# Performance work log

Measured on AMD Instinct MI355X. Metric: run time of the kernel, lower is better.

## Reference

```python
import jax, jax.numpy as jnp
import numpy as np

B, N, DIM, H = 8, 4096, 768, 12
HD = DIM // H
SCALE = HD ** -0.5


def setup_inputs() -> dict:
    key = jax.random.key(0)
    ks = jax.random.split(key, 6)
    x = jax.random.normal(ks[0], (B, N, DIM), dtype=jnp.float32)
    # torch nn.Linear weights: [out_features, in_features]
    Wqkv = jax.random.normal(ks[1], (3 * DIM, DIM), dtype=jnp.float32) * (DIM ** -0.5)
    Wp = jax.random.normal(ks[2], (DIM, DIM), dtype=jnp.float32) * (DIM ** -0.5)
    bp = jnp.zeros((DIM,), dtype=jnp.float32)
    w_q = jax.random.normal(ks[3], (H, HD), dtype=jnp.float32)
    w_k = jax.random.normal(ks[4], (H, HD), dtype=jnp.float32)
    return {"x": x, "Wqkv": Wqkv, "Wp": Wp, "bp": bp, "w_q": w_q, "w_k": w_k}


def reference(x, Wqkv, Wp, bp, w_q, w_k):
    b, n, c = x.shape
    qkv = x @ Wqkv.T                                   # [B,N,3C]
    # rearrange 'B N (qkv H C) -> qkv B H N C'
    qkv = qkv.reshape(b, n, 3, H, HD).transpose(2, 0, 3, 1, 4)
    q, k, v = qkv[0], qkv[1], qkv[2]                   # each [B,H,N,hd]

    alpha = jnp.einsum('bhnc,hc->bhn', q, w_q) * SCALE
    alpha = jax.nn.softmax(alpha, axis=-1)             # [B,H,N]
    global_q = jnp.einsum('bhn,bhnc->bhc', alpha, q)   # [B,H,hd]

    p = global_q[:, :, None, :] * k                    # [B,H,N,hd]
    beta = jnp.einsum('bhnc,hc->bhn', p, w_k) * SCALE
    beta = jax.nn.softmax(beta, axis=-1)
    global_k = jnp.einsum('bhn,bhnc->bhc', beta, k)    # [B,H,hd]

    u = global_k[:, :, None, :] * v                    # [B,H,N,hd]
    q_flat = q.transpose(0, 2, 1, 3).reshape(b, n, c)  # 'B H N C -> B N (H C)'
    u_flat = u.transpose(0, 2, 1, 3).reshape(b, n, c)
    return u_flat @ Wp.T + bp + q_flat
```

## Files before the change

kernel.cpp:

```cpp
#include <hip/hip_runtime.h>
#include <hip/hip_bf16.h>
#include <cstdint>
#include <cstddef>

#define B_ 8
#define N_ 4096
#define DIM_ 768
#define H_ 12
#define M_ (B_*N_)
#define SCALE_ 0.125f
#define KDIM 768
#define NKT 12
#define NITER 6

typedef __attribute__((ext_vector_type(8))) short s8v;
typedef __attribute__((ext_vector_type(4))) float f4v;

__device__ inline float bf2f(unsigned short u) {
    unsigned v = ((unsigned)u) << 16;
    return __builtin_bit_cast(float, v);
}
__device__ inline unsigned short f2bf(float f) {
    unsigned u = __builtin_bit_cast(unsigned, f);
    return (unsigned short)((u + 0x7FFFu + ((u >> 16) & 1u)) >> 16);
}
__device__ inline void gload16(const void* g, void* l) {
    __builtin_amdgcn_global_load_lds(
        (const __attribute__((address_space(1))) void*)g,
        (__attribute__((address_space(3))) void*)l, 16, 0, 0);
}

#define BARX() __builtin_amdgcn_s_barrier()
#define PRIO1() __builtin_amdgcn_s_setprio(1)
#define PRIO0() __builtin_amdgcn_s_setprio(0)
#define VM4() asm volatile("s_waitcnt vmcnt(4)" ::: "memory")
#define VM0() asm volatile("s_waitcnt vmcnt(0)" ::: "memory")

template<int PATH>
__global__ __launch_bounds__(512, 2)
void score_pass(const unsigned short* __restrict__ xb,
                const unsigned short* __restrict__ Vmat,
                float* __restrict__ pv, float* __restrict__ pms)
{
    __shared__ __align__(16) char smem[110592];
    const int tid = threadIdx.x;
    const int l = tid & 63, w = tid >> 6;
    const int lr = l & 15, g = l >> 4;

    const int nwg = gridDim.x, cpx = nwg >> 3;
    const int bid = blockIdx.x;
    const int tm = (bid & 7) * cpx + (bid >> 3);
    const int m0 = tm * 256;
    const int b = m0 >> 12;
    const int slice = (m0 & (N_ - 1)) >> 8;

    const long ldaB = (long)KDIM * 2;
    const int srA = w * 8 + (l >> 3);
    const int kbs = (l & 7) * 16;
    const int kbx = kbs ^ ((srA & 7) << 4);
    long offA[2];
    offA[0] = (long)(srA) * ldaB + kbx;
    offA[1] = (long)(128 + srA) * ldaB + kbx;

    const char* Abase = (const char*)(xb + (size_t)m0 * KDIM);
    const char* Vbase = (const char*)Vmat + (PATH ? (size_t)b * 16 * KDIM * 2 : 0);

    const int kx0 = (g * 16) ^ ((lr & 7) << 4);
    const int kx1 = (64 + g * 16) ^ ((lr & 7) << 4);

#define STG_A(buf_, qm_, kt_) { \
    const char* s0_ = Abase + (long)(kt_) * 2 + (long)(qm_) * 64 * ldaB; \
    char* d0_ = smem + ((buf_) * 4 + (qm_)) * 16384 + w * 1024; \
    gload16(s0_ + offA[0], d0_); \
    gload16(s0_ + offA[1], d0_ + 8192); }

    if (w < 2) {
        const int rw = l >> 3;
        const int by = ((l & 7) * 16) ^ (rw << 4);
#pragma unroll
        for (int k6 = 0; k6 < 6; ++k6) {
            const int kt = w * 6 + k6;
            gload16(Vbase + (size_t)rw * 1536 + kt * 128 + by,
                    smem + 32768 + kt * 2048);
            gload16(Vbase + (size_t)(8 + rw) * 1536 + kt * 128 + by,
                    smem + 32768 + kt * 2048 + 1024);
        }
    }
    STG_A(0, 0, 0); STG_A(0, 1, 0);
    STG_A(1, 0, 64); STG_A(1, 1, 64);
    VM4(); BARX();

    f4v sacc[2] = {};
    for (int kt = 0; kt < 12; ++kt) {
        const int buf = kt & 1;
#pragma unroll
        for (int j = 0; j < 2; ++j) {
            const int r0 = w * 32 + j * 16;
            const int qm = (r0 >> 6) & 1, hi = r0 >> 7, loc = r0 & 63;
            const char* ab = smem + (buf * 4 + qm) * 16384 + hi * 8192 + (loc + lr) * 128;
            s8v a0 = *(const s8v*)(ab + kx0);
            s8v a1 = *(const s8v*)(ab + kx1);
            const char* vb = smem + 32768 + kt * 2048 + lr * 128;
            s8v b0 = *(const s8v*)(vb + kx0);
            s8v b1 = *(const s8v*)(vb + kx1);
            sacc[j] = __builtin_amdgcn_mfma_f32_16x16x32_bf16(a0, b0, sacc[j], 0, 0, 0);
            sacc[j] = __builtin_amdgcn_mfma_f32_16x16x32_bf16(a1, b1, sacc[j], 0, 0, 0);
        }
        BARX();
        if (kt + 2 < 12) {
            const int kk2 = (kt + 2) * 64;
            STG_A(buf, 0, kk2); STG_A(buf, 1, kk2);
        }
        if (kt <= 9) { VM4(); } else { VM0(); }
        BARX();
    }

    float dd[8];
#pragma unroll
    for (int j = 0; j < 2; ++j)
#pragma unroll
        for (int r = 0; r < 4; ++r) dd[j * 4 + r] = sacc[j][r] * SCALE_;

    float mw = dd[0];
#pragma unroll
    for (int q2 = 1; q2 < 8; ++q2) mw = fmaxf(mw, dd[q2]);
    mw = fmaxf(mw, __shfl_xor(mw, 16));
    mw = fmaxf(mw, __shfl_xor(mw, 32));
    float* Lm = (float*)(smem + 107008);
    float* Ls = (float*)(smem + 107520);
    if (l < 16) Lm[w * 16 + lr] = mw;
    __syncthreads();
    float mfin = Lm[lr];
#pragma unroll
    for (int w2 = 1; w2 < 8; ++w2) mfin = fmaxf(mfin, Lm[w2 * 16 + lr]);

    float ss = 0.f;
#pragma unroll
    for (int j = 0; j < 2; ++j)
#pragma unroll
        for (int r = 0; r < 4; ++r) {
            const float e = __expf(dd[j * 4 + r] - mfin);
            ss += e;
            const int row = w * 32 + j * 16 + g * 4 + r;
            *(unsigned short*)(smem + 98304 + lr * 544 + row * 2) = f2bf(e);
        }
    ss += __shfl_xor(ss, 16);
    ss += __shfl_xor(ss, 32);
    if (l < 16) Ls[w * 16 + lr] = ss;
    __syncthreads();

    if (tid < 12) {
        float S = 0.f;
#pragma unroll
        for (int w2 = 0; w2 < 8; ++w2) S += Ls[w2 * 16 + tid];
        float M2 = Lm[tid];
#pragma unroll
        for (int w2 = 1; w2 < 8; ++w2) M2 = fmaxf(M2, Lm[w2 * 16 + tid]);
        pms[((size_t)(b * H_ + tid) * 16 + slice) * 2 + 0] = M2;
        pms[((size_t)(b * H_ + tid) * 16 + slice) * 2 + 1] = S;
    }
    __syncthreads();

    for (int it = 0; it < 6; ++it) {
        const int ktA = it * 2, ktB = it * 2 + 1;
        STG_A(0, 0, ktA * 64); STG_A(0, 1, ktA * 64);
        STG_A(1, 0, ktB * 64); STG_A(1, 1, ktB * 64);
        VM0(); BARX();
        const int buf = w >> 2;
        const int kt = it * 2 + buf;
        const int d0 = (w & 3) * 16;
        const int dby = (d0 + (l & 15)) * 2;
        f4v pacc = {};
#pragma unroll
        for (int c = 0; c < 8; ++c) {
            s8v ae = *(const s8v*)(smem + 98304 + (l & 15) * 544
                                   + (c * 32 + (l >> 4) * 8) * 2);
            const char* xr = smem + (buf * 4 + ((c >> 1) & 1)) * 16384 + (c >> 2) * 8192;
            const int nb = (c & 1) * 32 + (l >> 4) * 8;
            s8v bx;
#pragma unroll
            for (int j = 0; j < 8; ++j)
                bx[j] = (short)*(const unsigned short*)(xr + (nb + j) * 128 + (dby ^ (j << 4)));
            pacc = __builtin_amdgcn_mfma_f32_16x16x32_bf16(ae, bx, pacc, 0, 0, 0);
        }
        if ((l >> 4) < 3) {
#pragma unroll
            for (int r = 0; r < 4; ++r) {
                const int h = (l >> 4) * 4 + r;
                pv[((size_t)(b * 16 + slice) * 12 + h) * 768
                   + kt * 64 + d0 + (l & 15)] = pacc[r];
            }
        }
        BARX();
    }
#undef STG_A
}

template<int MODE>
__global__ __launch_bounds__(512, 2)
void gemm128(const unsigned short* __restrict__ A, int ldaE,
             const unsigned short* __restrict__ Bmat,
             float* __restrict__ Cf, unsigned short* __restrict__ CbO,
             const float* __restrict__ bias, const float* __restrict__ addW,
             int Nc, int ntn)
{
    __shared__ __align__(16) char smem[98304];
    const int tid = threadIdx.x;
    const int l = tid & 63, w = tid >> 6;
    const int lr = l & 15, g = l >> 4;
    const int wm = w >> 2, wn = w & 3;

    const int nwg = gridDim.x, cpx = nwg >> 3;
    const int bid = blockIdx.x;
    const int lg = (bid & 7) * cpx + (bid >> 3);
    const int tm = lg / ntn, tn = lg % ntn;
    const int m0 = tm * 128, n0 = tn * 256;

    const long ldaB = (long)ldaE * 2;
    const long ldbB = (long)KDIM * 2;

    const unsigned short* Bp = Bmat;
    if (MODE == 0) Bp = Bmat + (size_t)(m0 >> 12) * (DIM_ * DIM_);

    const int srA = w * 8 + (l >> 3);
    const int kbs = (l & 7) * 16;
    const int kbx = kbs ^ ((srA & 7) << 4);
    long offA[2], offB[2];
    offA[0] = (long)(srA) * ldaB + kbx;
    offA[1] = (long)(64 + srA) * ldaB + kbx;
    offB[0] = (long)(((srA >> 5)) * 64 + (srA & 31)) * ldbB + kbx;
    offB[1] = (long)((2 + (srA >> 5)) * 64 + (srA & 31)) * ldbB + kbx;

    const char* Abase = (const char*)(A + (size_t)m0 * ldaE);
    const char* Bbase = (const char*)(Bp + (size_t)n0 * KDIM);

    const int aoff = (wm * 64 + lr) * 128;
    const int boff = (wn * 32 + lr) * 128;
    const int kx0 = (g * 16) ^ ((lr & 7) << 4);
    const int kx1 = (64 + g * 16) ^ ((lr & 7) << 4);

    f4v acc[4][4] = {};
    s8v af[4][2];
    s8v bfr[2][2][2];

#define STG_A1(buf_, kt_) { \
    const char* s0_ = Abase + (long)(kt_) * 2; \
    char* d0_ = smem + ((buf_) * 3) * 16384 + w * 1024; \
    gload16(s0_ + offA[0], d0_); \
    gload16(s0_ + offA[1], d0_ + 8192); }

#define STG_B1(buf_, qn_, kt_) { \
    const char* s0_ = Bbase + (long)(kt_) * 2 + (long)(qn_) * 32 * ldbB; \
    char* d0_ = smem + ((buf_) * 3 + 1 + (qn_)) * 16384 + w * 1024; \
    gload16(s0_ + offB[0], d0_); \
    gload16(s0_ + offB[1], d0_ + 8192); }

#define DS_A1(buf_) { \
    const char* ba_ = smem + ((buf_) * 3) * 16384 + aoff; \
    af[0][0] = *(const s8v*)(ba_ +    0 + kx0); af[0][1] = *(const s8v*)(ba_ +    0 + kx1); \
    af[1][0] = *(const s8v*)(ba_ + 2048 + kx0); af[1][1] = *(const s8v*)(ba_ + 2048 + kx1); \
    af[2][0] = *(const s8v*)(ba_ + 4096 + kx0); af[2][1] = *(const s8v*)(ba_ + 4096 + kx1); \
    af[3][0] = *(const s8v*)(ba_ + 6144 + kx0); af[3][1] = *(const s8v*)(ba_ + 6144 + kx1); }

#define DS_B1(buf_, qn_) { \
    const char* bb_ = smem + ((buf_) * 3 + 1 + (qn_)) * 16384 + boff; \
    bfr[qn_][0][0] = *(const s8v*)(bb_ +    0 + kx0); bfr[qn_][0][1] = *(const s8v*)(bb_ +    0 + kx1); \
    bfr[qn_][1][0] = *(const s8v*)(bb_ + 2048 + kx0); bfr[qn_][1][1] = *(const s8v*)(bb_ + 2048 + kx1); }

#define MM1(fm_, fng_, qn_, kk_) \
    acc[fm_][fng_] = __builtin_amdgcn_mfma_f32_16x16x32_bf16(af[fm_][kk_], bfr[qn_][(fng_)&1][kk_], acc[fm_][fng_], 0, 0, 0);

#define MFMA16_1(qn_, kk_) \
    MM1(0, (qn_)*2+0, qn_, kk_) MM1(0, (qn_)*2+1, qn_, kk_) \
    MM1(1, (qn_)*2+0, qn_, kk_) MM1(1, (qn_)*2+1, qn_, kk_) \
    MM1(2, (qn_)*2+0, qn_, kk_) MM1(2, (qn_)*2+1, qn_, kk_) \
    MM1(3, (qn_)*2+0, qn_, kk_) MM1(3, (qn_)*2+1, qn_, kk_)

#define MFMA32_1(qn_) { MFMA16_1(qn_, 0) MFMA16_1(qn_, 1) }

    STG_A1(0, 0); STG_B1(0, 0, 0); STG_B1(0, 1, 0);
    STG_A1(1, 64); STG_B1(1, 0, 64);
    VM4(); BARX();

    for (int i = 0; i < NITER; ++i) {
        const int t1k = (2 * i + 1) * 64, t2k = (2 * i + 2) * 64, t3k = (2 * i + 3) * 64;
        const bool h2 = (2 * i + 2) < NKT, h3 = (2 * i + 3) < NKT;
        const bool last = (i == NITER - 1);
        DS_A1(0); DS_B1(0, 0); STG_B1(1, 1, t1k);
        BARX(); PRIO1(); MFMA32_1(0); PRIO0(); BARX();
        DS_B1(0, 1); if (h2) { STG_A1(0, t2k); STG_B1(0, 0, t2k); }
        BARX(); PRIO1(); MFMA32_1(1); PRIO0();
        if (last) { VM0(); } else { VM4(); }
        BARX();
        DS_A1(1); DS_B1(1, 0); if (h2) STG_B1(0, 1, t2k);
        BARX(); PRIO1(); MFMA32_1(0); PRIO0(); BARX();
        DS_B1(1, 1); if (h3) { STG_A1(1, t3k); STG_B1(1, 0, t3k); }
        BARX(); PRIO1(); MFMA32_1(1); PRIO0();
        if (last) { VM0(); } else { VM4(); }
        BARX();
    }

    const int jb = m0 % DIM_;
#pragma unroll
    for (int fm = 0; fm < 4; ++fm) {
#pragma unroll
        for (int fng = 0; fng < 4; ++fng) {
            const int col = n0 + wn * 64 + fng * 16 + lr;
#pragma unroll
            for (int r = 0; r < 4; ++r) {
                const int ro = wm * 64 + fm * 16 + g * 4 + r;
                const int row = m0 + ro;
                if (MODE == 0) {
                    Cf[(size_t)row * Nc + col] = acc[fm][fng][r] + bias[col];
                } else {
                    CbO[(size_t)row * Nc + col] =
                        f2bf(acc[fm][fng][r] + addW[(size_t)(jb + ro) * DIM_ + col]);
                }
            }
        }
    }
#undef STG_A1
#undef STG_B1
#undef DS_A1
#undef DS_B1
#undef MM1
#undef MFMA16_1
#undef MFMA32_1
}

__global__ __launch_bounds__(256)
void reduce_a(const float* __restrict__ pv1, const float* __restrict__ pms1,
              const float* __restrict__ Wqkv, const float* __restrict__ w_k,
              unsigned short* __restrict__ bvecs)
{
    const int b = blockIdx.x / H_, h = blockIdx.x % H_;
    const int t = threadIdx.x;
    const int w = t >> 6, l = t & 63;
    __shared__ float Svec[768];
    __shared__ float ew[16];
    __shared__ float Ssh;
    __shared__ float gqwk[64];

    const float* pp = pms1 + (size_t)(b * H_ + h) * 16 * 2;
    float M = pp[0];
    for (int s = 1; s < 16; ++s) M = fmaxf(M, pp[s * 2]);
    if (t < 16) ew[t] = __expf(pp[t * 2] - M);
    __syncthreads();
    if (t == 0) {
        float S = 0.f;
        for (int s = 0; s < 16; ++s) S += ew[s] * pp[s * 2 + 1];
        Ssh = S;
    }
#pragma unroll
    for (int j = 0; j < 3; ++j) {
        const int col = t + j * 256;
        float v = 0.f;
        for (int s = 0; s < 16; ++s)
            v += ew[s] * pv1[((size_t)(b * 16 + s) * 12 + h) * 768 + col];
        Svec[col] = v;
    }
    __syncthreads();

    const float invS = 1.f / Ssh;
    for (int i = 0; i < 16; ++i) {
        const int o = w * 16 + i;
        const float* wr = Wqkv + (size_t)(h * 64 + o) * 768;
        float s = 0.f;
#pragma unroll
        for (int j = 0; j < 12; ++j)
            s += wr[l + j * 64] * Svec[l + j * 64];
        s += __shfl_xor(s, 1); s += __shfl_xor(s, 2); s += __shfl_xor(s, 4);
        s += __shfl_xor(s, 8); s += __shfl_xor(s, 16); s += __shfl_xor(s, 32);
        if (l == 0) gqwk[o] = (s * invS) * w_k[h * 64 + o];
    }
    __syncthreads();

#pragma unroll
    for (int j = 0; j < 3; ++j) {
        const int dcol = t + j * 256;
        float bv = 0.f;
        for (int c = 0; c < 64; ++c)
            bv += gqwk[c] * Wqkv[(size_t)(DIM_ + h * 64 + c) * 768 + dcol];
        bvecs[(size_t)(b * 16 + h) * 768 + dcol] = f2bf(bv);
        if (h < 4) bvecs[(size_t)(b * 16 + 12 + h) * 768 + dcol] = 0;
    }
}

__global__ __launch_bounds__(256)
void reduce_b(const float* __restrict__ pv2, const float* __restrict__ pms2,
              const float* __restrict__ Wqkv, float* __restrict__ gkv)
{
    const int b = blockIdx.x / H_, h = blockIdx.x % H_;
    const int t = threadIdx.x;
    const int w = t >> 6, l = t & 63;
    __shared__ float Svec[768];
    __shared__ float ew[16];
    __shared__ float Ssh;

    const float* pp = pms2 + (size_t)(b * H_ + h) * 16 * 2;
    float M = pp[0];
    for (int s = 1; s < 16; ++s) M = fmaxf(M, pp[s * 2]);
    if (t < 16) ew[t] = __expf(pp[t * 2] - M);
    __syncthreads();
    if (t == 0) {
        float S = 0.f;
        for (int s = 0; s < 16; ++s) S += ew[s] * pp[s * 2 + 1];
        Ssh = S;
    }
#pragma unroll
    for (int j = 0; j < 3; ++j) {
        const int col = t + j * 256;
        float v = 0.f;
        for (int s = 0; s < 16; ++s)
            v += ew[s] * pv2[((size_t)(b * 16 + s) * 12 + h) * 768 + col];
        Svec[col] = v;
    }
    __syncthreads();

    const float invS = 1.f / Ssh;
    for (int i = 0; i < 16; ++i) {
        const int o = w * 16 + i;
        const float* wr = Wqkv + (size_t)(DIM_ + h * 64 + o) * 768;
        float s = 0.f;
#pragma unroll
        for (int j = 0; j < 12; ++j)
            s += wr[l + j * 64] * Svec[l + j * 64];
        s += __shfl_xor(s, 1); s += __shfl_xor(s, 2); s += __shfl_xor(s, 4);
        s += __shfl_xor(s, 8); s += __shfl_xor(s, 16); s += __shfl_xor(s, 32);
        if (l == 0) gkv[(size_t)b * DIM_ + h * 64 + o] = s * invS;
    }
}

__global__ __launch_bounds__(256)
void avec_prep(const float* __restrict__ Wqkv, const float* __restrict__ w_q,
               unsigned short* __restrict__ avecb)
{
    const int h = blockIdx.x;
    const int t = threadIdx.x;
    if (h >= H_) {
#pragma unroll
        for (int j = 0; j < 3; ++j) avecb[(size_t)h * 768 + t + j * 256] = 0;
        return;
    }
    __shared__ float wl[64];
    if (t < 64) wl[t] = w_q[h * 64 + t];
    __syncthreads();
#pragma unroll
    for (int j = 0; j < 3; ++j) {
        const int dcol = t + j * 256;
        float a = 0.f;
        for (int c = 0; c < 64; ++c)
            a += wl[c] * Wqkv[(size_t)(h * 64 + c) * 768 + dcol];
        avecb[(size_t)h * 768 + dcol] = f2bf(a);
    }
}

__global__ void cvt_all(const float* __restrict__ x, const float* __restrict__ Wqkv,
                        unsigned short* __restrict__ xb, unsigned short* __restrict__ wvT,
                        int n4x)
{
    int i = blockIdx.x * 256 + threadIdx.x;
    if (i < n4x) {
        float4 v = ((const float4*)x)[i];
        ushort4 o;
        o.x = f2bf(v.x); o.y = f2bf(v.y); o.z = f2bf(v.z); o.w = f2bf(v.w);
        ((ushort4*)xb)[i] = o;
    } else {
        const int k = i - n4x;
        const int ii = k % DIM_;
        const int c0 = (k / DIM_) * 4;
        ushort4 o;
        o.x = f2bf(Wqkv[(size_t)(2 * DIM_ + c0 + 0) * DIM_ + ii]);
        o.y = f2bf(Wqkv[(size_t)(2 * DIM_ + c0 + 1) * DIM_ + ii]);
        o.z = f2bf(Wqkv[(size_t)(2 * DIM_ + c0 + 2) * DIM_ + ii]);
        o.w = f2bf(Wqkv[(size_t)(2 * DIM_ + c0 + 3) * DIM_ + ii]);
        *(ushort4*)&wvT[(size_t)ii * DIM_ + c0] = o;
    }
}

__global__ __launch_bounds__(256)
void fold_wp(const float* __restrict__ Wp, const float* __restrict__ gk,
             unsigned short* __restrict__ W2)
{
    int idx = blockIdx.x * 256 + threadIdx.x;
    int e4 = idx * 4;
    int b = (int)((unsigned)e4 / (unsigned)(DIM_ * DIM_));
    int rem = e4 - b * (DIM_ * DIM_);
    int c = rem % DIM_;
    float4 wv = *(const float4*)&Wp[rem];
    const float* gp = &gk[b * DIM_ + c];
    ushort4 o;
    o.x = f2bf(wv.x * gp[0]); o.y = f2bf(wv.y * gp[1]);
    o.z = f2bf(wv.z * gp[2]); o.w = f2bf(wv.w * gp[3]);
    *(ushort4*)&W2[e4] = o;
}

extern "C" void kernel_launch(void* const* d_in, const int* in_sizes, int n_in,
                              void* d_out, int out_size, void* d_ws, size_t ws_size,
                              hipStream_t stream)
{
    const float* x    = (const float*)d_in[0];
    const float* Wqkv = (const float*)d_in[1];
    const float* Wp   = (const float*)d_in[2];
    const float* bp   = (const float*)d_in[3];
    const float* w_q  = (const float*)d_in[4];
    const float* w_k  = (const float*)d_in[5];
    float* out = (float*)d_out;

    constexpr size_t NXB = (size_t)M_ * DIM_;
    constexpr size_t NWV = (size_t)DIM_ * DIM_;
    constexpr size_t NW2 = (size_t)B_ * DIM_ * DIM_;

    char* p = (char*)d_ws;
    unsigned short* xb    = (unsigned short*)p; p += NXB * 2;
    unsigned short* wvT   = (unsigned short*)p; p += NWV * 2;
    unsigned short* w2b   = (unsigned short*)p; p += NW2 * 2;
    unsigned short* w4b   = (unsigned short*)p; p += NW2 * 2;
    unsigned short* avecb = (unsigned short*)p; p += (size_t)16 * 768 * 2;
    unsigned short* bvecs = (unsigned short*)p; p += (size_t)B_ * 16 * 768 * 2;
    float* pv1  = (float*)p; p += (size_t)B_ * 16 * 12 * 768 * 4;
    float* pms1 = (float*)p; p += (size_t)B_ * H_ * 16 * 2 * 4;
    float* pv2  = (float*)p; p += (size_t)B_ * 16 * 12 * 768 * 4;
    float* pms2 = (float*)p; p += (size_t)B_ * H_ * 16 * 2 * 4;
    float* gkv  = (float*)p; p += (size_t)B_ * DIM_ * 4;

    constexpr int N4X  = (int)(NXB / 4);
    constexpr int NTOT = N4X + (int)(NWV / 4);
    cvt_all<<<NTOT / 256, 256, 0, stream>>>(x, Wqkv, xb, wvT, N4X);

    avec_prep<<<16, 256, 0, stream>>>(Wqkv, w_q, avecb);

    score_pass<0><<<128, 512, 0, stream>>>(xb, avecb, pv1, pms1);

    reduce_a<<<B_ * H_, 256, 0, stream>>>(pv1, pms1, Wqkv, w_k, bvecs);

    score_pass<1><<<128, 512, 0, stream>>>(xb, bvecs, pv2, pms2);

    reduce_b<<<B_ * H_, 256, 0, stream>>>(pv2, pms2, Wqkv, gkv);

    fold_wp<<<(int)(NW2 / 4 / 256), 256, 0, stream>>>(Wp, gkv, w2b);

    gemm128<1><<<48 * 3, 512, 0, stream>>>(w2b, DIM_, wvT, nullptr, w4b, nullptr, Wqkv,
                                           DIM_, 3);

    gemm128<0><<<256 * 3, 512, 0, stream>>>(xb, DIM_, w4b, out, nullptr, bp, nullptr,
                                            DIM_, 3);
}
```

Baseline: 199.9 us.

## Halve score_pass row tile to 128 and fold avec_prep into cvt_all

score_pass now handles 128 rows per workgroup instead of 256, launching 256 workgroups instead of 128. This fills more CUs and shrinks shared memory from about 108KB to 64KB, which may allow more resident workgroups. The partial-result buffers and the reduce kernels are resized from 16 to 32 slices per batch, which doubles the partial-reduction traffic. avec_prep is merged into cvt_all as extra blocks, removing one kernel launch.

After: 200.2 us. About the same (+0.1%).

```diff
diff --git a/kernel.cpp b/kernel.cpp
--- a/kernel.cpp
+++ b/kernel.cpp
@@ -34,7 +34,12 @@
 #define PRIO1() __builtin_amdgcn_s_setprio(1)
 #define PRIO0() __builtin_amdgcn_s_setprio(0)
 #define VM4() asm volatile("s_waitcnt vmcnt(4)" ::: "memory")
+#define VM2() asm volatile("s_waitcnt vmcnt(2)" ::: "memory")
 #define VM0() asm volatile("s_waitcnt vmcnt(0)" ::: "memory")
+
+#define EOFF 57344
+#define LMOFF 62976
+#define LSOFF 63488
 
 template<int PATH>
 __global__ __launch_bounds__(512, 2)
@@ -42,7 +47,7 @@
                 const unsigned short* __restrict__ Vmat,
                 float* __restrict__ pv, float* __restrict__ pms)
 {
-    __shared__ __align__(16) char smem[110592];
+    __shared__ __align__(16) char smem[64000];
     const int tid = threadIdx.x;
     const int l = tid & 63, w = tid >> 6;
     const int lr = l & 15, g = l >> 4;
@@ -50,9 +55,9 @@
     const int nwg = gridDim.x, cpx = nwg >> 3;
     const int bid = blockIdx.x;
     const int tm = (bid & 7) * cpx + (bid >> 3);
-    const int m0 = tm * 256;
+    const int m0 = tm * 128;
     const int b = m0 >> 12;
-    const int slice = (m0 & (N_ - 1)) >> 8;
+    const int slice = (m0 & (N_ - 1)) >> 7;
 
     const long ldaB = (long)KDIM * 2;
     const int srA = w * 8 + (l >> 3);
@@ -60,7 +65,7 @@
     const int kbx = kbs ^ ((srA & 7) << 4);
     long offA[2];
     offA[0] = (long)(srA) * ldaB + kbx;
-    offA[1] = (long)(128 + srA) * ldaB + kbx;
+    offA[1] = (long)(64 + srA) * ldaB + kbx;
 
     const char* Abase = (const char*)(xb + (size_t)m0 * KDIM);
     const char* Vbase = (const char*)Vmat + (PATH ? (size_t)b * 16 * KDIM * 2 : 0);
@@ -68,9 +73,9 @@
     const int kx0 = (g * 16) ^ ((lr & 7) << 4);
     const int kx1 = (64 + g * 16) ^ ((lr & 7) << 4);
 
-#define STG_A(buf_, qm_, kt_) { \
-    const char* s0_ = Abase + (long)(kt_) * 2 + (long)(qm_) * 64 * ldaB; \
-    char* d0_ = smem + ((buf_) * 4 + (qm_)) * 16384 + w * 1024; \
+#define STG_A(buf_, kt_) { \
+    const char* s0_ = Abase + (long)(kt_) * 2; \
+    char* d0_ = smem + (buf_) * 16384 + w * 1024; \
     gload16(s0_ + offA[0], d0_); \
     gload16(s0_ + offA[1], d0_ + 8192); }
 
@@ -86,48 +91,38 @@
                     smem + 32768 + kt * 2048 + 1024);
         }
     }
-    STG_A(0, 0, 0); STG_A(0, 1, 0);
-    STG_A(1, 0, 64); STG_A(1, 1, 64);
-    VM4(); BARX();
-
-    f4v sacc[2] = {};
+    STG_A(0, 0); STG_A(1, 64);
+    VM2(); BARX();
+
+    f4v sacc = {};
+    const int hi1 = w >> 2, loc1 = (w & 3) * 16;
     for (int kt = 0; kt < 12; ++kt) {
         const int buf = kt & 1;
-#pragma unroll
-        for (int j = 0; j < 2; ++j) {
-            const int r0 = w * 32 + j * 16;
-            const int qm = (r0 >> 6) & 1, hi = r0 >> 7, loc = r0 & 63;
-            const char* ab = smem + (buf * 4 + qm) * 16384 + hi * 8192 + (loc + lr) * 128;
+        {
+            const char* ab = smem + buf * 16384 + hi1 * 8192 + (loc1 + lr) * 128;
             s8v a0 = *(const s8v*)(ab + kx0);
             s8v a1 = *(const s8v*)(ab + kx1);
             const char* vb = smem + 32768 + kt * 2048 + lr * 128;
             s8v b0 = *(const s8v*)(vb + kx0);
             s8v b1 = *(const s8v*)(vb + kx1);
-            sacc[j] = __builtin_amdgcn_mfma_f32_16x16x32_bf16(a0, b0, sacc[j], 0, 0, 0);
-            sacc[j] = __builtin_amdgcn_mfma_f32_16x16x32_bf16(a1, b1, sacc[j], 0, 0, 0);
+            sacc = __builtin_amdgcn_mfma_f32_16x16x32_bf16(a0, b0, sacc, 0, 0, 0);
+            sacc = __builtin_amdgcn_mfma_f32_16x16x32_bf16(a1, b1, sacc, 0, 0, 0);
         }
         BARX();
-        if (kt + 2 < 12) {
-            const int kk2 = (kt + 2) * 64;
-            STG_A(buf, 0, kk2); STG_A(buf, 1, kk2);
-        }
-        if (kt <= 9) { VM4(); } else { VM0(); }
+        if (kt + 2 < 12) STG_A(buf, (kt + 2) * 64);
+        if (kt <= 9) { VM2(); } else { VM0(); }
         BARX();
     }
 
-    float dd[8];
-#pragma unroll
-    for (int j = 0; j < 2; ++j)
-#pragma unroll
-        for (int r = 0; r < 4; ++r) dd[j * 4 + r] = sacc[j][r] * SCALE_;
-
-    float mw = dd[0];
-#pragma unroll
-    for (int q2 = 1; q2 < 8; ++q2) mw = fmaxf(mw, dd[q2]);
+    float dd[4];
+#pragma unroll
+    for (int r = 0; r < 4; ++r) dd[r] = sacc[r] * SCALE_;
+
+    float mw = fmaxf(fmaxf(dd[0], dd[1]), fmaxf(dd[2], dd[3]));
     mw = fmaxf(mw, __shfl_xor(mw, 16));
     mw = fmaxf(mw, __shfl_xor(mw, 32));
-    float* Lm = (float*)(smem + 107008);
-    float* Ls = (float*)(smem + 107520);
+    float* Lm = (float*)(smem + LMOFF);
+    float* Ls = (float*)(smem + LSOFF);
     if (l < 16) Lm[w * 16 + lr] = mw;
     __syncthreads();
     float mfin = Lm[lr];
@@ -136,14 +131,12 @@
 
     float ss = 0.f;
 #pragma unroll
-    for (int j = 0; j < 2; ++j)
-#pragma unroll
-        for (int r = 0; r < 4; ++r) {
-            const float e = __expf(dd[j * 4 + r] - mfin);
-            ss += e;
-            const int row = w * 32 + j * 16 + g * 4 + r;
-            *(unsigned short*)(smem + 98304 + lr * 544 + row * 2) = f2bf(e);
-        }
+    for (int r = 0; r < 4; ++r) {
+        const float e = __expf(dd[r] - mfin);
+        ss += e;
+        const int row = w * 16 + g * 4 + r;
+        *(unsigned short*)(smem + EOFF + lr * 352 + row * 2) = f2bf(e);
+    }
     ss += __shfl_xor(ss, 16);
     ss += __shfl_xor(ss, 32);
     if (l < 16) Ls[w * 16 + lr] = ss;
@@ -156,15 +149,14 @@
         float M2 = Lm[tid];
 #pragma unroll
         for (int w2 = 1; w2 < 8; ++w2) M2 = fmaxf(M2, Lm[w2 * 16 + tid]);
-        pms[((size_t)(b * H_ + tid) * 16 + slice) * 2 + 0] = M2;
-        pms[((size_t)(b * H_ + tid) * 16 + slice) * 2 + 1] = S;
+        pms[((size_t)(b * H_ + tid) * 32 + slice) * 2 + 0] = M2;
+        pms[((size_t)(b * H_ + tid) * 32 + slice) * 2 + 1] = S;
     }
     __syncthreads();
 
     for (int it = 0; it < 6; ++it) {
-        const int ktA = it * 2, ktB = it * 2 + 1;
-        STG_A(0, 0, ktA * 64); STG_A(0, 1, ktA * 64);
-        STG_A(1, 0, ktB * 64); STG_A(1, 1, ktB * 64);
+        STG_A(0, (it * 2) * 64);
+        STG_A(1, (it * 2 + 1) * 64);
         VM0(); BARX();
         const int buf = w >> 2;
         const int kt = it * 2 + buf;
@@ -172,10 +164,10 @@
         const int dby = (d0 + (l & 15)) * 2;
         f4v pacc = {};
 #pragma unroll
-        for (int c = 0; c < 8; ++c) {
-            s8v ae = *(const s8v*)(smem + 98304 + (l & 15) * 544
+        for (int c = 0; c < 4; ++c) {
+            s8v ae = *(const s8v*)(smem + EOFF + (l & 15) * 352
                                    + (c * 32 + (l >> 4) * 8) * 2);
-            const char* xr = smem + (buf * 4 + ((c >> 1) & 1)) * 16384 + (c >> 2) * 8192;
+            const char* xr = smem + buf * 16384 + (c >> 1) * 8192;
             const int nb = (c & 1) * 32 + (l >> 4) * 8;
             s8v bx;
 #pragma unroll
@@ -187,7 +179,7 @@
 #pragma unroll
             for (int r = 0; r < 4; ++r) {
                 const int h = (l >> 4) * 4 + r;
-                pv[((size_t)(b * 16 + slice) * 12 + h) * 768
+                pv[((size_t)(b * 32 + slice) * 12 + h) * 768
                    + kt * 64 + d0 + (l & 15)] = pacc[r];
             }
         }
@@ -337,26 +329,26 @@
     const int t = threadIdx.x;
     const int w = t >> 6, l = t & 63;
     __shared__ float Svec[768];
-    __shared__ float ew[16];
+    __shared__ float ew[32];
     __shared__ float Ssh;
     __shared__ float gqwk[64];
 
-    const float* pp = pms1 + (size_t)(b * H_ + h) * 16 * 2;
+    const float* pp = pms1 + (size_t)(b * H_ + h) * 32 * 2;
     float M = pp[0];
-    for (int s = 1; s < 16; ++s) M = fmaxf(M, pp[s * 2]);
-    if (t < 16) ew[t] = __expf(pp[t * 2] - M);
+    for (int s = 1; s < 32; ++s) M = fmaxf(M, pp[s * 2]);
+    if (t < 32) ew[t] = __expf(pp[t * 2] - M);
     __syncthreads();
     if (t == 0) {
         float S = 0.f;
-        for (int s = 0; s < 16; ++s) S += ew[s] * pp[s * 2 + 1];
+        for (int s = 0; s < 32; ++s) S += ew[s] * pp[s * 2 + 1];
         Ssh = S;
     }
 #pragma unroll
     for (int j = 0; j < 3; ++j) {
         const int col = t + j * 256;
         float v = 0.f;
-        for (int s = 0; s < 16; ++s)
-            v += ew[s] * pv1[((size_t)(b * 16 + s) * 12 + h) * 768 + col];
+        for (int s = 0; s < 32; ++s)
+            v += ew[s] * pv1[((size_t)(b * 32 + s) * 12 + h) * 768 + col];
         Svec[col] = v;
     }
     __syncthreads();
@@ -394,25 +386,25 @@
     const int t = threadIdx.x;
     const int w = t >> 6, l = t & 63;
     __shared__ float Svec[768];
-    __shared__ float ew[16];
+    __shared__ float ew[32];
     __shared__ float Ssh;
 
-    const float* pp = pms2 + (size_t)(b * H_ + h) * 16 * 2;
+    const float* pp = pms2 + (size_t)(b * H_ + h) * 32 * 2;
     float M = pp[0];
-    for (int s = 1; s < 16; ++s) M = fmaxf(M, pp[s * 2]);
-    if (t < 16) ew[t] = __expf(pp[t * 2] - M);
+    for (int s = 1; s < 32; ++s) M = fmaxf(M, pp[s * 2]);
+    if (t < 32) ew[t] = __expf(pp[t * 2] - M);
     __syncthreads();
     if (t == 0) {
         float S = 0.f;
-        for (int s = 0; s < 16; ++s) S += ew[s] * pp[s * 2 + 1];
+        for (int s = 0; s < 32; ++s) S += ew[s] * pp[s * 2 + 1];
         Ssh = S;
     }
 #pragma unroll
     for (int j = 0; j < 3; ++j) {
         const int col = t + j * 256;
         float v = 0.f;
-        for (int s = 0; s < 16; ++s)
-            v += ew[s] * pv2[((size_t)(b * 16 + s) * 12 + h) * 768 + col];
+        for (int s = 0; s < 32; ++s)
+            v += ew[s] * pv2[((size_t)(b * 32 + s) * 12 + h) * 768 + col];
         Svec[col] = v;
     }
     __syncthreads();
@@ -431,34 +423,33 @@
     }
 }
 
-__global__ __launch_bounds__(256)
-void avec_prep(const float* __restrict__ Wqkv, const float* __restrict__ w_q,
-               unsigned short* __restrict__ avecb)
-{
-    const int h = blockIdx.x;
-    const int t = threadIdx.x;
-    if (h >= H_) {
-#pragma unroll
-        for (int j = 0; j < 3; ++j) avecb[(size_t)h * 768 + t + j * 256] = 0;
+__global__ void cvt_all(const float* __restrict__ x, const float* __restrict__ Wqkv,
+                        const float* __restrict__ w_q,
+                        unsigned short* __restrict__ xb, unsigned short* __restrict__ wvT,
+                        unsigned short* __restrict__ avecb,
+                        int n4x, int nblk_cvt)
+{
+    if ((int)blockIdx.x >= nblk_cvt) {
+        const int h = blockIdx.x - nblk_cvt;
+        const int t = threadIdx.x;
+        if (h >= H_) {
+#pragma unroll
+            for (int j = 0; j < 3; ++j) avecb[(size_t)h * 768 + t + j * 256] = 0;
+            return;
+        }
+        __shared__ float wl[64];
+        if (t < 64) wl[t] = w_q[h * 64 + t];
+        __syncthreads();
+#pragma unroll
+        for (int j = 0; j < 3; ++j) {
+            const int dcol = t + j * 256;
+            float a = 0.f;
+            for (int c = 0; c < 64; ++c)
+                a += wl[c] * Wqkv[(size_t)(h * 64 + c) * 768 + dcol];
+            avecb[(size_t)h * 768 + dcol] = f2bf(a);
+        }
         return;
     }
-    __shared__ float wl[64];
-    if (t < 64) wl[t] = w_q[h * 64 + t];
-    __syncthreads();
-#pragma unroll
-    for (int j = 0; j < 3; ++j) {
-        const int dcol = t + j * 256;
-        float a = 0.f;
-        for (int c = 0; c < 64; ++c)
-            a += wl[c] * Wqkv[(size_t)(h * 64 + c) * 768 + dcol];
-        avecb[(size_t)h * 768 + dcol] = f2bf(a);
-    }
-}
-
-__global__ void cvt_all(const float* __restrict__ x, const float* __restrict__ Wqkv,
-                        unsigned short* __restrict__ xb, unsigned short* __restrict__ wvT,
-                        int n4x)
-{
     int i = blockIdx.x * 256 + threadIdx.x;
     if (i < n4x) {
         float4 v = ((const float4*)x)[i];
@@ -518,23 +509,21 @@
     unsigned short* w4b   = (unsigned short*)p; p += NW2 * 2;
     unsigned short* avecb = (unsigned short*)p; p += (size_t)16 * 768 * 2;
     unsigned short* bvecs = (unsigned short*)p; p += (size_t)B_ * 16 * 768 * 2;
-    float* pv1  = (float*)p; p += (size_t)B_ * 16 * 12 * 768 * 4;
-    float* pms1 = (float*)p; p += (size_t)B_ * H_ * 16 * 2 * 4;
-    float* pv2  = (float*)p; p += (size_t)B_ * 16 * 12 * 768 * 4;
-    float* pms2 = (float*)p; p += (size_t)B_ * H_ * 16 * 2 * 4;
+    float* pv1  = (float*)p; p += (size_t)B_ * 32 * 12 * 768 * 4;
+    float* pms1 = (float*)p; p += (size_t)B_ * H_ * 32 * 2 * 4;
+    float* pv2  = (float*)p; p += (size_t)B_ * 32 * 12 * 768 * 4;
+    float* pms2 = (float*)p; p += (size_t)B_ * H_ * 32 * 2 * 4;
     float* gkv  = (float*)p; p += (size_t)B_ * DIM_ * 4;
 
     constexpr int N4X  = (int)(NXB / 4);
-    constexpr int NTOT = N4X + (int)(NWV / 4);
-    cvt_all<<<NTOT / 256, 256, 0, stream>>>(x, Wqkv, xb, wvT, N4X);
-
-    avec_prep<<<16, 256, 0, stream>>>(Wqkv, w_q, avecb);
-
-    score_pass<0><<<128, 512, 0, stream>>>(xb, avecb, pv1, pms1);
+    constexpr int NBLK = (N4X + (int)(NWV / 4)) / 256;
+    cvt_all<<<NBLK + 16, 256, 0, stream>>>(x, Wqkv, w_q, xb, wvT, avecb, N4X, NBLK);
+
+    score_pass<0><<<256, 512, 0, stream>>>(xb, avecb, pv1, pms1);
 
     reduce_a<<<B_ * H_, 256, 0, stream>>>(pv1, pms1, Wqkv, w_k, bvecs);
 
-    score_pass<1><<<128, 512, 0, stream>>>(xb, bvecs, pv2, pms2);
+    score_pass<1><<<256, 512, 0, stream>>>(xb, bvecs, pv2, pms2);
 
     reduce_b<<<B_ * H_, 256, 0, stream>>>(pv2, pms2, Wqkv, gkv);
 
```
